# Kernel optimization log

Hardware: AMD Instinct MI355X
Metric: run time of the kernel (lower is better)

## Reference

```python
import jax, jax.numpy as jnp
import numpy as np

B, D, C, W, H = 2, 8, 256, 84, 84
NUM_HEADS = 8
WS = (2, 7, 7)
SS = (1, 3, 3)
MLP_RATIO = 4
EPS = 1e-5


def _rel_pos_index(ws):
    # static int index table (N, N), matches WindowAttention3D buffer
    coords = np.stack(np.meshgrid(np.arange(ws[0]), np.arange(ws[1]), np.arange(ws[2]), indexing='ij'))
    cf = coords.reshape(3, -1)
    rel = (cf[:, :, None] - cf[:, None, :]).transpose(1, 2, 0).copy()
    rel[:, :, 0] += ws[0] - 1
    rel[:, :, 1] += ws[1] - 1
    rel[:, :, 2] += ws[2] - 1
    rel[:, :, 0] *= (2 * ws[1] - 1) * (2 * ws[2] - 1)
    rel[:, :, 1] *= 2 * ws[2] - 1
    return rel.sum(-1)


def _attn_mask(Dp, Hp, Wp, ws, ss):
    # static additive shift mask (nW, N, N), matches create_mask
    m = np.zeros((Dp, Hp, Wp))
    cnt = 0
    for d in (slice(0, -ws[0]), slice(-ws[0], -ss[0]), slice(-ss[0], None)):
        for h in (slice(0, -ws[1]), slice(-ws[1], -ss[1]), slice(-ss[1], None)):
            for w in (slice(0, -ws[2]), slice(-ws[2], -ss[2]), slice(-ss[2], None)):
                m[d, h, w] = cnt
                cnt += 1
    mw = m.reshape(Dp // ws[0], ws[0], Hp // ws[1], ws[1], Wp // ws[2], ws[2])
    mw = mw.transpose(0, 2, 4, 1, 3, 5).reshape(-1, ws[0] * ws[1] * ws[2])
    diff = mw[:, None, :] - mw[:, :, None]
    return np.where(diff != 0, -100.0, 0.0).astype(np.float32)


def _layernorm(x, g, b):
    mu = x.mean(-1, keepdims=True)
    var = ((x - mu) ** 2).mean(-1, keepdims=True)
    return (x - mu) * jax.lax.rsqrt(var + EPS) * g + b


def setup_inputs():
    key = jax.random.key(0)
    ks = jax.random.split(key, 6)
    hidden = C * MLP_RATIO
    nbias = (2 * WS[0] - 1) * (2 * WS[1] - 1) * (2 * WS[2] - 1)
    s = lambda k, shape, sc=0.02: jax.random.normal(k, shape, jnp.float32) * sc
    return dict(
        x=jax.random.normal(ks[0], (B, D, C, W, H), jnp.float32),
        norm1_g=jnp.ones((C,), jnp.float32), norm1_b=jnp.zeros((C,), jnp.float32),
        qkv_w=s(ks[1], (3 * C, C)),
        rpb_table=s(ks[2], (nbias, NUM_HEADS)),
        proj_w=s(ks[3], (C, C)), proj_b=jnp.zeros((C,), jnp.float32),
        norm2_g=jnp.ones((C,), jnp.float32), norm2_b=jnp.zeros((C,), jnp.float32),
        fc1_w=s(ks[4], (hidden, C)), fc1_b=jnp.zeros((hidden,), jnp.float32),
        fc2_w=s(ks[5], (C, hidden)), fc2_b=jnp.zeros((C,), jnp.float32),
    )


def reference(x, norm1_g, norm1_b, qkv_w, rpb_table, proj_w, proj_b,
              norm2_g, norm2_b, fc1_w, fc1_b, fc2_w, fc2_b):
    # x: (B, D, C, W, H) -> (B, D, H, W, C)
    xp = jnp.transpose(x, (0, 1, 4, 3, 2))
    Bn, Dn, Hn, Wn, Cn = xp.shape
    wd, wh, ww = WS
    N = wd * wh * ww
    nW = (Dn // wd) * (Hn // wh) * (Wn // ww)
    head_dim = Cn // NUM_HEADS
    scale = head_dim ** -0.5

    rel_idx = _rel_pos_index(WS)                      # (N, N) static
    mask = jnp.asarray(_attn_mask(Dn, Hn, Wn, WS, SS))  # (nW, N, N) static

    shortcut = xp
    h1 = _layernorm(xp, norm1_g, norm1_b)
    # cyclic shift (D,H,W divisible by window -> no padding)
    h1 = jnp.roll(h1, shift=(-SS[0], -SS[1], -SS[2]), axis=(1, 2, 3))
    # window partition -> (B*nW, N, C)
    xw = h1.reshape(Bn, Dn // wd, wd, Hn // wh, wh, Wn // ww, ww, Cn)
    xw = jnp.transpose(xw, (0, 1, 3, 5, 2, 4, 6, 7)).reshape(-1, N, Cn)
    B_ = xw.shape[0]

    qkv = (xw @ qkv_w.T).reshape(B_, N, 3, NUM_HEADS, head_dim)
    qkv = jnp.transpose(qkv, (2, 0, 3, 1, 4))  # (3, B_, h, N, hd)
    q, k, v = qkv[0] * scale, qkv[1], qkv[2]
    attn = jnp.einsum('bhnd,bhmd->bhnm', q, k)
    bias = rpb_table[rel_idx.reshape(-1)].reshape(N, N, NUM_HEADS)
    attn = attn + jnp.transpose(bias, (2, 0, 1))[None]
    attn = attn.reshape(Bn, nW, NUM_HEADS, N, N) + mask[None, :, None]
    attn = jax.nn.softmax(attn.reshape(B_, NUM_HEADS, N, N), axis=-1)
    out = jnp.einsum('bhnm,bhmd->bhnd', attn, v)
    out = jnp.transpose(out, (0, 2, 1, 3)).reshape(B_, N, Cn)
    out = out @ proj_w.T + proj_b

    # window reverse -> (B, D, H, W, C)
    out = out.reshape(Bn, Dn // wd, Hn // wh, Wn // ww, wd, wh, ww, Cn)
    out = jnp.transpose(out, (0, 1, 4, 2, 5, 3, 6, 7)).reshape(Bn, Dn, Hn, Wn, Cn)
    out = jnp.roll(out, shift=(SS[0], SS[1], SS[2]), axis=(1, 2, 3))

    xres = shortcut + out
    # MLP block (torch GELU = exact erf)
    h2 = _layernorm(xres, norm2_g, norm2_b)
    h2 = jax.nn.gelu(h2 @ fc1_w.T + fc1_b, approximate=False)
    h2 = h2 @ fc2_w.T + fc2_b
    y = xres + h2
    return jnp.transpose(y, (0, 1, 4, 3, 2))  # back to (B, D, C, W, H)
```

## Files before the change

kernel.cpp:

```cpp
#include <hip/hip_runtime.h>
#include <hip/hip_bf16.h>
#include <cstdint>
#include <cstddef>

#define B_   2
#define D_   8
#define C_   256
#define W_   84
#define H_   84
#define NH   8
#define HD   32
#define NTOK 98
#define WH   7056
#define M2   56448
#define NWC  576

typedef __attribute__((ext_vector_type(8))) short sh8;
typedef __attribute__((ext_vector_type(4))) float f32x4;
typedef __hip_bfloat16 bf16;

#define AS1 __attribute__((address_space(1)))
#define AS3 __attribute__((address_space(3)))

__global__ __launch_bounds__(256) void k_f2b(const float* __restrict__ in,
                                             bf16* __restrict__ out, int n) {
  int i = blockIdx.x * 256 + threadIdx.x;
  if (i < n) out[i] = __float2bfloat16(in[i]);
}

__global__ __launch_bounds__(256) void k_bias(const float* __restrict__ rpb,
                                              float* __restrict__ tbl) {
  int cls = blockIdx.x >> 3, h = blockIdx.x & 7;
  int dB = cls >> 2, hB = (cls >> 1) & 1, wB = cls & 1;
  for (int idx = threadIdx.x; idx < 112 * 112; idx += 256) {
    int r = idx / 112, c = idx - (idx / 112) * 112;
    int rt = r < 98 ? r : 97, ct = c < 98 ? c : 97;
    int jdr = rt / 49, remr = rt % 49, jhr = remr / 7, jwr = remr % 7;
    int jdc = ct / 49, remc = ct % 49, jhc = remc / 7, jwc = remc % 7;
    int bir = jdr * 169 + jhr * 13 + jwr, bic = jdc * 169 + jhc * 13 + jwc;
    int dgr = dB ? ((6 + jdr) < 7 ? 1 : 2) : 0;
    int hgr = hB ? ((77 + jhr) < 81 ? 1 : 2) : 0;
    int wgr = wB ? ((77 + jwr) < 81 ? 1 : 2) : 0;
    int dgc = dB ? ((6 + jdc) < 7 ? 1 : 2) : 0;
    int hgc = hB ? ((77 + jhc) < 81 ? 1 : 2) : 0;
    int wgc = wB ? ((77 + jwc) < 81 ? 1 : 2) : 0;
    int cir = dgr * 9 + hgr * 3 + wgr, cic = dgc * 9 + hgc * 3 + wgc;
    float v = rpb[(bir - bic + 253) * 8 + h] + (cir == cic ? 0.f : -100.f);
    tbl[((size_t)(cls * 8 + h) * 112 + r) * 112 + c] = v;
  }
}

__device__ __forceinline__ int inv_row(int b, int d0, int w0, int h0) {
  int sd = (d0 + 7) & 7;
  int lid = (sd >> 1) & 1, jd = sd & 1;
  int sh = h0 + 81; if (sh >= 84) sh -= 84;
  int sw = w0 + 81; if (sw >= 84) sw -= 84;
  int ih = sh / 7, jh = sh - ih * 7;
  int iw = sw / 7, jw = sw - iw * 7;
  return (b * 288 + lid * 144 + ih * 12 + iw) * 98 + jd * 49 + jh * 7 + jw;
}

__global__ __launch_bounds__(256) void k_xpose_w(const float* __restrict__ x,
                                                 float* __restrict__ xtw, int cchunk) {
  int blk = blockIdx.x;
  int ch = blk & 1;
  int t = blk >> 1;
  int w0 = t % 84;
  int t2 = t / 84;
  int i = t2 & 3, b = t2 >> 2;
  int d0 = (cchunk * 4 + 1 + i) & 7;
  __shared__ float tile[128][85];
  __shared__ int rtab[84];
  int tid = threadIdx.x;
  if (tid < 84) rtab[tid] = inv_row(b, d0, w0, tid);
  const float* src = x + ((size_t)(b * 8 + d0) * 256 + ch * 128) * WH + w0 * 84;
  for (int idx = tid; idx < 128 * 21; idx += 256) {
    int c = idx / 21, h4 = idx - c * 21;
    float4 v = *(const float4*)(src + (size_t)c * WH + h4 * 4);
    tile[c][h4 * 4 + 0] = v.x; tile[c][h4 * 4 + 1] = v.y;
    tile[c][h4 * 4 + 2] = v.z; tile[c][h4 * 4 + 3] = v.w;
  }
  __syncthreads();
  for (int idx = tid; idx < 84 * 128; idx += 256) {
    int h = idx >> 7, cc = idx & 127;
    xtw[(size_t)rtab[h] * 256 + ch * 128 + cc] = tile[cc][h];
  }
}

__global__ __launch_bounds__(256) void k_ln1_lin(
    const float* __restrict__ xtw, const float* __restrict__ g,
    const float* __restrict__ bb, bf16* __restrict__ xw) {
  int rl = blockIdx.x * 4 + (threadIdx.x >> 6);
  int lane = threadIdx.x & 63;
  int c0 = lane * 4;
  float4 v = *(const float4*)(xtw + (size_t)rl * 256 + c0);
  float s = v.x + v.y + v.z + v.w;
  float s2 = v.x * v.x + v.y * v.y + v.z * v.z + v.w * v.w;
#pragma unroll
  for (int off = 32; off; off >>= 1) { s += __shfl_xor(s, off, 64); s2 += __shfl_xor(s2, off, 64); }
  float mu = s * (1.f / 256.f);
  float var = s2 * (1.f / 256.f) - mu * mu;
  float rs = rsqrtf(var + 1e-5f);
  float4 gg = *(const float4*)(g + c0);
  float4 bv = *(const float4*)(bb + c0);
  bf16 tmp[4];
  tmp[0] = __float2bfloat16((v.x - mu) * rs * gg.x + bv.x);
  tmp[1] = __float2bfloat16((v.y - mu) * rs * gg.y + bv.y);
  tmp[2] = __float2bfloat16((v.z - mu) * rs * gg.z + bv.z);
  tmp[3] = __float2bfloat16((v.w - mu) * rs * gg.w + bv.w);
  *(ushort4*)(&xw[(size_t)rl * 256 + c0]) = *(ushort4*)tmp;
}

__device__ __forceinline__ float gelu_fast(float v) {
  float x = v * 0.70710678118f;
  float ax = fabsf(x);
  float t = 1.0f / (1.0f + 0.3275911f * ax);
  float y = t * (0.254829592f + t * (-0.284496736f +
            t * (1.421413741f + t * (-1.453152027f + t * 1.061405429f))));
  float er = 1.0f - y * __expf(-ax * ax);
  er = copysignf(er, x);
  return 0.5f * v * (1.0f + er);
}

template <int EPI, int NK>
__global__ __launch_bounds__(256) void k_gemm_bt(
    const bf16* __restrict__ A, const bf16* __restrict__ Bw,
    int M, int N,
    const float* __restrict__ bias, const float* __restrict__ res,
    void* __restrict__ outv) {
  constexpr int K = NK * 32;
  __shared__ __align__(16) short smem[16384];
  int nwg = gridDim.x;
  int orig = blockIdx.x;
  int q8 = nwg >> 3, r8 = nwg & 7;
  int xcd = orig & 7, lwg = orig >> 3;
  int bid = (xcd < r8 ? xcd * (q8 + 1) : r8 * (q8 + 1) + (xcd - r8) * q8) + lwg;
  int nbn = N >> 7;
  int bm = bid / nbn, bn = bid - bm * nbn;
  int tid = threadIdx.x;
  int lane = tid & 63, wv = tid >> 6;
  int wr = wv >> 1, wc = wv & 1;
  f32x4 acc[4][4] = {};
  const short* Ag = (const short*)A + (size_t)bm * 128 * K;
  const short* Bg = (const short*)Bw + (size_t)bn * 128 * K;
  int rIn = lane >> 2;
  int cSrc = ((lane & 3) ^ ((lane >> 3) & 3)) * 8;
  const short* gA0 = Ag + (size_t)(wv * 32 + rIn) * K + cSrc;
  const short* gA1 = gA0 + 16 * K;
  const short* gB0 = Bg + (size_t)(wv * 32 + rIn) * K + cSrc;
  const short* gB1 = gB0 + 16 * K;
  const int ldsW = wv * 1024;
  int rb = wr * 64 + (lane & 15);
  int cb = wc * 64 + (lane & 15);
  int kswz = ((lane >> 4) ^ ((lane >> 1) & 3)) * 8;
  const short* rdA = smem + rb * 32 + kswz;
  const short* rdB = smem + 4096 + cb * 32 + kswz;

  __builtin_amdgcn_global_load_lds((const AS1 void*)gA0, (AS3 void*)&smem[ldsW], 16, 0, 0);
  __builtin_amdgcn_global_load_lds((const AS1 void*)gA1, (AS3 void*)&smem[ldsW + 512], 16, 0, 0);
  __builtin_amdgcn_global_load_lds((const AS1 void*)gB0, (AS3 void*)&smem[4096 + ldsW], 16, 0, 0);
  __builtin_amdgcn_global_load_lds((const AS1 void*)gB1, (AS3 void*)&smem[4096 + ldsW + 512], 16, 0, 0);

#pragma unroll
  for (int kt = 0; kt < NK; ++kt) {
    const int buf = kt & 1;
    __builtin_amdgcn_s_barrier();
    if (kt + 1 < NK) {
      const int wb = (buf ^ 1) * 8192;
      __builtin_amdgcn_global_load_lds((const AS1 void*)(gA0 + (kt + 1) * 32),
                                       (AS3 void*)&smem[wb + ldsW], 16, 0, 0);
      __builtin_amdgcn_global_load_lds((const AS1 void*)(gA1 + (kt + 1) * 32),
                                       (AS3 void*)&smem[wb + ldsW + 512], 16, 0, 0);
      __builtin_amdgcn_global_load_lds((const AS1 void*)(gB0 + (kt + 1) * 32),
                                       (AS3 void*)&smem[wb + 4096 + ldsW], 16, 0, 0);
      __builtin_amdgcn_global_load_lds((const AS1 void*)(gB1 + (kt + 1) * 32),
                                       (AS3 void*)&smem[wb + 4096 + ldsW + 512], 16, 0, 0);
      asm volatile("s_waitcnt vmcnt(4)" ::: "memory");
    } else {
      asm volatile("s_waitcnt vmcnt(0)" ::: "memory");
    }
    __builtin_amdgcn_s_barrier();
    __builtin_amdgcn_sched_barrier(0);
    sh8 af[4], bfr[4];
#pragma unroll
    for (int m = 0; m < 4; ++m) af[m] = *(const sh8*)(rdA + buf * 8192 + m * 512);
#pragma unroll
    for (int n2 = 0; n2 < 4; ++n2) bfr[n2] = *(const sh8*)(rdB + buf * 8192 + n2 * 512);
    __builtin_amdgcn_s_setprio(1);
#pragma unroll
    for (int m = 0; m < 4; ++m)
#pragma unroll
      for (int n2 = 0; n2 < 4; ++n2)
        acc[m][n2] = __builtin_amdgcn_mfma_f32_16x16x32_bf16(af[m], bfr[n2], acc[m][n2], 0, 0, 0);
    __builtin_amdgcn_s_setprio(0);
  }
  int rbase = bm * 128 + wr * 64 + ((lane >> 4) << 2);
  int cbase = bn * 128 + wc * 64 + (lane & 15);
#pragma unroll
  for (int m = 0; m < 4; ++m) {
#pragma unroll
    for (int j = 0; j < 4; ++j) {
      int r = rbase + m * 16 + j;
#pragma unroll
      for (int n2 = 0; n2 < 4; ++n2) {
        int cc = cbase + n2 * 16;
        float v = acc[m][n2][j];
        if (EPI == 2) {
          v += bias[cc] + res[(size_t)r * N + cc];
          ((float*)outv)[(size_t)r * N + cc] = v;
        } else {
          if (bias) v += bias[cc];
          if (EPI == 1) v = gelu_fast(v);
          ((bf16*)outv)[(size_t)r * N + cc] = __float2bfloat16(v);
        }
      }
    }
  }
}

__global__ __launch_bounds__(64) void k_attn_mfma(
    const bf16* __restrict__ qkv, const float* __restrict__ tbl,
    bf16* __restrict__ aout, int idbase) {
  int blk = blockIdx.x;
  int wl = blk >> 3, h = blk & 7;
  int lid = (wl / 144) & 1;
  int id = idbase + lid;
  int rem = wl % 144;
  int ih = rem / 12, iw = rem - ih * 12;
  int cls = ((id == 3) ? 4 : 0) + ((ih == 11) ? 2 : 0) + ((iw == 11) ? 1 : 0);
  const float* bt = tbl + (size_t)(cls * 8 + h) * 112 * 112;
  int lane = threadIdx.x;
  __shared__ __align__(16) short vt[32][136];
  __shared__ __align__(16) short pb[16][136];
  sh8 z = {};
  for (int i = lane; i < 544; i += 64) *((sh8*)&vt[0][0] + i) = z;
  for (int i = lane; i < 272; i += 64) *((sh8*)&pb[0][0] + i) = z;
  __syncthreads();
  const size_t base = (size_t)wl * NTOK * 768;
  for (int i = lane; i < 98 * 8; i += 64) {
    int c = i >> 3, d4 = (i & 7) * 4;
    ushort4 vu = *(const ushort4*)&qkv[base + (size_t)c * 768 + 512 + h * 32 + d4];
    vt[d4 + 0][c] = (short)vu.x; vt[d4 + 1][c] = (short)vu.y;
    vt[d4 + 2][c] = (short)vu.z; vt[d4 + 3][c] = (short)vu.w;
  }
  int kq = (lane >> 4) * 8;
  sh8 kf[7];
#pragma unroll
  for (int jt = 0; jt < 7; ++jt) {
    int c = jt * 16 + (lane & 15);
    kf[jt] = *(const sh8*)&qkv[base + (size_t)c * 768 + 256 + h * 32 + kq];
  }
  __syncthreads();
  sh8 vb[2][4];
#pragma unroll
  for (int dt = 0; dt < 2; ++dt)
#pragma unroll
    for (int k2 = 0; k2 < 4; ++k2)
      vb[dt][k2] = *(const sh8*)&vt[dt * 16 + (lane & 15)][k2 * 32 + kq];

  const float scale = 0.17677669529663687f;
  f32x4 zc = {};
  int rband = (lane >> 4) * 4;
  for (int it = 0; it < 7; ++it) {
    int rq = it * 16 + (lane & 15);
    sh8 qf = *(const sh8*)&qkv[base + (size_t)rq * 768 + h * 32 + kq];
    f32x4 s[7];
#pragma unroll
    for (int jt = 0; jt < 7; ++jt)
      s[jt] = __builtin_amdgcn_mfma_f32_16x16x32_bf16(qf, kf[jt], zc, 0, 0, 0);
    float p[7][4], linv[4];
#pragma unroll
    for (int j = 0; j < 4; ++j) {
      int r2 = it * 16 + rband + j;
      float rs = 0.f;
#pragma unroll
      for (int jt = 0; jt < 7; ++jt) {
        int c = jt * 16 + (lane & 15);
        float v = s[jt][j] * scale + bt[r2 * 112 + c];
        float e = __expf(v);
        if (jt == 6 && (lane & 15) >= 2) e = 0.f;
        p[jt][j] = e;
        rs += e;
      }
      rs += __shfl_xor(rs, 1, 64); rs += __shfl_xor(rs, 2, 64);
      rs += __shfl_xor(rs, 4, 64); rs += __shfl_xor(rs, 8, 64);
      linv[j] = 1.f / rs;
    }
#pragma unroll
    for (int j = 0; j < 4; ++j)
#pragma unroll
      for (int jt = 0; jt < 7; ++jt) {
        bf16 bv = __float2bfloat16(p[jt][j] * linv[j]);
        pb[rband + j][jt * 16 + (lane & 15)] = *(short*)&bv;
      }
    __syncthreads();
    sh8 pa[4];
#pragma unroll
    for (int k2 = 0; k2 < 4; ++k2)
      pa[k2] = *(const sh8*)&pb[lane & 15][k2 * 32 + kq];
    f32x4 o[2] = {};
#pragma unroll
    for (int dt = 0; dt < 2; ++dt)
#pragma unroll
      for (int k2 = 0; k2 < 4; ++k2)
        o[dt] = __builtin_amdgcn_mfma_f32_16x16x32_bf16(pa[k2], vb[dt][k2], o[dt], 0, 0, 0);
#pragma unroll
    for (int j = 0; j < 4; ++j) {
      int r2 = it * 16 + rband + j;
      if (r2 < 98) {
#pragma unroll
        for (int dt = 0; dt < 2; ++dt) {
          bf16 ov = __float2bfloat16(o[dt][j]);
          aout[((size_t)wl * 98 + r2) * 256 + h * 32 + dt * 16 + (lane & 15)] = ov;
        }
      }
    }
    __syncthreads();
  }
}

__global__ __launch_bounds__(256) void k_xres_ln2_lin(
    const float* __restrict__ xtw, const bf16* __restrict__ pout,
    const float* __restrict__ g, const float* __restrict__ bb,
    float* __restrict__ xres, bf16* __restrict__ ln2) {
  int rl = blockIdx.x * 4 + (threadIdx.x >> 6);
  int lane = threadIdx.x & 63;
  int c0 = lane * 4;
  float4 v = *(const float4*)(xtw + (size_t)rl * 256 + c0);
  ushort4 pu = *(const ushort4*)(pout + (size_t)rl * 256 + c0);
  v.x += __bfloat162float(*(bf16*)&pu.x);
  v.y += __bfloat162float(*(bf16*)&pu.y);
  v.z += __bfloat162float(*(bf16*)&pu.z);
  v.w += __bfloat162float(*(bf16*)&pu.w);
  *(float4*)(xres + (size_t)rl * 256 + c0) = v;
  float s = v.x + v.y + v.z + v.w;
  float s2 = v.x * v.x + v.y * v.y + v.z * v.z + v.w * v.w;
#pragma unroll
  for (int off = 32; off; off >>= 1) { s += __shfl_xor(s, off, 64); s2 += __shfl_xor(s2, off, 64); }
  float mu = s * (1.f / 256.f);
  float var = s2 * (1.f / 256.f) - mu * mu;
  float rs = rsqrtf(var + 1e-5f);
  float4 gg = *(const float4*)(g + c0);
  float4 bv = *(const float4*)(bb + c0);
  bf16 tmp[4];
  tmp[0] = __float2bfloat16((v.x - mu) * rs * gg.x + bv.x);
  tmp[1] = __float2bfloat16((v.y - mu) * rs * gg.y + bv.y);
  tmp[2] = __float2bfloat16((v.z - mu) * rs * gg.z + bv.z);
  tmp[3] = __float2bfloat16((v.w - mu) * rs * gg.w + bv.w);
  *(ushort4*)(&ln2[(size_t)rl * 256 + c0]) = *(ushort4*)tmp;
}

__global__ __launch_bounds__(256) void k_final_c(const float* __restrict__ y,
                                                 float* __restrict__ out, int cchunk) {
  int t = blockIdx.x;
  int w0 = t % 84;
  int t2 = t / 84;
  int i = t2 & 3, b = t2 >> 2;
  int d0 = (cchunk * 4 + 1 + i) & 7;
  __shared__ float tile[84][65];
  __shared__ int rtab[84];
  int tid = threadIdx.x;
  if (tid < 84) rtab[tid] = inv_row(b, d0, w0, tid);
  __syncthreads();
  for (int c0 = 0; c0 < 256; c0 += 64) {
    for (int idx = tid; idx < 84 * 64; idx += 256) {
      int hh = idx >> 6, cc = idx & 63;
      tile[hh][cc] = y[(size_t)rtab[hh] * 256 + c0 + cc];
    }
    __syncthreads();
    for (int idx = tid; idx < 64 * 84; idx += 256) {
      int cc = idx / 84, hh = idx - cc * 84;
      out[((((size_t)b * 8 + d0) * 256 + c0 + cc) * 84 + w0) * 84 + hh] = tile[hh][cc];
    }
    __syncthreads();
  }
}

extern "C" void kernel_launch(void* const* d_in, const int* in_sizes, int n_in,
                              void* d_out, int out_size, void* d_ws, size_t ws_size,
                              hipStream_t stream) {
  const float* x      = (const float*)d_in[0];
  const float* n1g    = (const float*)d_in[1];
  const float* n1b    = (const float*)d_in[2];
  const float* qkv_w  = (const float*)d_in[3];
  const float* rpb    = (const float*)d_in[4];
  const float* proj_w = (const float*)d_in[5];
  const float* proj_b = (const float*)d_in[6];
  const float* n2g    = (const float*)d_in[7];
  const float* n2b    = (const float*)d_in[8];
  const float* fc1_w  = (const float*)d_in[9];
  const float* fc1_b  = (const float*)d_in[10];
  const float* fc2_w  = (const float*)d_in[11];
  const float* fc2_b  = (const float*)d_in[12];
  float* out = (float*)d_out;

  char* w = (char*)d_ws;
  size_t off = 0;
  bf16* wq = (bf16*)(w + off); off += (size_t)768 * 256 * 2;
  bf16* wp = (bf16*)(w + off); off += (size_t)256 * 256 * 2;
  bf16* w1 = (bf16*)(w + off); off += (size_t)1024 * 256 * 2;
  bf16* w2 = (bf16*)(w + off); off += (size_t)1024 * 256 * 2;
  float* tbl = (float*)(w + off); off += (size_t)8 * 8 * 112 * 112 * 4;

  float* xtw  = (float*)(w + off); off += (size_t)M2 * 1024;
  bf16*  xw   = (bf16*)(w + off);  off += (size_t)M2 * 512;
  char*  qreg = w + off;           off += (size_t)M2 * 1536;
  float* xres = (float*)(w + off); off += (size_t)M2 * 1024;
  bf16*  hid  = (bf16*)(w + off);
  bf16* qkvb = (bf16*)qreg;
  bf16* aout = xw;
  bf16* pout = (bf16*)qreg;
  bf16* ln2b = (bf16*)(qreg + (size_t)M2 * 512);
  float* ybuf = xtw;

  int subTiles = 21;
  if (off + (size_t)441 * 128 * 2048 + 1024 <= ws_size) subTiles = 441;
  else if (off + (size_t)147 * 128 * 2048 + 1024 <= ws_size) subTiles = 147;
  else if (off + (size_t)49 * 128 * 2048 + 1024 <= ws_size) subTiles = 49;
  const int nsub = 441 / subTiles;
  const int MSUB = subTiles * 128;

  k_f2b<<<(196608 + 255) / 256, 256, 0, stream>>>(qkv_w, wq, 196608);
  k_f2b<<<(65536 + 255) / 256, 256, 0, stream>>>(proj_w, wp, 65536);
  k_f2b<<<(262144 + 255) / 256, 256, 0, stream>>>(fc1_w, w1, 262144);
  k_f2b<<<(262144 + 255) / 256, 256, 0, stream>>>(fc2_w, w2, 262144);
  k_bias<<<64, 256, 0, stream>>>(rpb, tbl);

  for (int c = 0; c < 2; ++c) {
    k_xpose_w<<<1344, 256, 0, stream>>>(x, xtw, c);
    k_ln1_lin<<<M2 / 4, 256, 0, stream>>>(xtw, n1g, n1b, xw);
    k_gemm_bt<0, 8><<<441 * 6, 256, 0, stream>>>(xw, wq, M2, 768, nullptr, nullptr, qkvb);
    k_attn_mfma<<<NWC * NH, 64, 0, stream>>>(qkvb, tbl, aout, 2 * c);
    k_gemm_bt<0, 8><<<441 * 2, 256, 0, stream>>>(aout, wp, M2, 256, proj_b, nullptr, pout);
    k_xres_ln2_lin<<<M2 / 4, 256, 0, stream>>>(xtw, pout, n2g, n2b, xres, ln2b);
    for (int s = 0; s < nsub; ++s) {
      size_t m0 = (size_t)s * MSUB;
      k_gemm_bt<1, 8><<<subTiles * 8, 256, 0, stream>>>(
          ln2b + m0 * 256, w1, MSUB, 1024, fc1_b, nullptr, hid);
      k_gemm_bt<2, 32><<<subTiles * 2, 256, 0, stream>>>(
          hid, w2, MSUB, 256, fc2_b, xres + m0 * 256, ybuf + m0 * 256);
    }
    k_final_c<<<672, 256, 0, stream>>>(ybuf, out, c);
  }
}
```

Baseline: 841.5 us.

## Add 128x256-tile 512-thread GEMM for QKV and FC1 projections

Introduces a new GEMM kernel using 512 threads (8 waves) with a 128x256 output tile, double-buffered direct global-to-LDS loads, swizzled LDS reads and XCD-aware block remapping. It replaces the older 128-wide-N GEMM for the QKV and FC1 projections so each A tile is reused across twice as many output columns, halving the number of A reloads. The larger tile raises LDS use to 48KB and register pressure, which may lower occupancy.

```diff
diff --git a/kernel.cpp b/kernel.cpp
--- a/kernel.cpp
+++ b/kernel.cpp
@@ -218,6 +218,94 @@
   }
 }
 
+template <int EPI, int NK>
+__global__ __launch_bounds__(512) void k_gemm_w(
+    const bf16* __restrict__ A, const bf16* __restrict__ Bw,
+    int M, int N,
+    const float* __restrict__ bias, const float* __restrict__ res,
+    void* __restrict__ outv) {
+  constexpr int K = NK * 32;
+  __shared__ __align__(16) short smem[24576];
+  int nwg = gridDim.x;
+  int orig = blockIdx.x;
+  int q8 = nwg >> 3, r8 = nwg & 7;
+  int xcd = orig & 7, lwg = orig >> 3;
+  int bid = (xcd < r8 ? xcd * (q8 + 1) : r8 * (q8 + 1) + (xcd - r8) * q8) + lwg;
+  int nbn = N >> 8;
+  int bm = bid / nbn, bn = bid - bm * nbn;
+  int tid = threadIdx.x;
+  int lane = tid & 63, wv = tid >> 6;
+  int wr = wv >> 2, wc = wv & 3;
+  f32x4 acc[4][4] = {};
+  const short* Ag = (const short*)A + (size_t)bm * 128 * K;
+  const short* Bg = (const short*)Bw + (size_t)bn * 256 * K;
+  int rIn = lane >> 2;
+  int cSrc = ((lane & 3) ^ ((lane >> 3) & 3)) * 8;
+  const short* gA0 = Ag + (size_t)(wv * 16 + rIn) * K + cSrc;
+  const short* gB0 = Bg + (size_t)(wv * 32 + rIn) * K + cSrc;
+  const short* gB1 = gB0 + 16 * K;
+  const int ldsA = wv * 512;
+  const int ldsB = 4096 + wv * 1024;
+  int rb = wr * 64 + (lane & 15);
+  int cb = wc * 64 + (lane & 15);
+  int kswz = ((lane >> 4) ^ ((lane >> 1) & 3)) * 8;
+  const short* rdA = smem + rb * 32 + kswz;
+  const short* rdB = smem + 4096 + cb * 32 + kswz;
+
+  __builtin_amdgcn_global_load_lds((const AS1 void*)gA0, (AS3 void*)&smem[ldsA], 16, 0, 0);
+  __builtin_amdgcn_global_load_lds((const AS1 void*)gB0, (AS3 void*)&smem[ldsB], 16, 0, 0);
+  __builtin_amdgcn_global_load_lds((const AS1 void*)gB1, (AS3 void*)&smem[ldsB + 512], 16, 0, 0);
+
+#pragma unroll
+  for (int kt = 0; kt < NK; ++kt) {
+    const int buf = kt & 1;
+    __builtin_amdgcn_s_barrier();
+    if (kt + 1 < NK) {
+      const int wb = (buf ^ 1) * 12288;
+      __builtin_amdgcn_global_load_lds((const AS1 void*)(gA0 + (kt + 1) * 32),
+                                       (AS3 void*)&smem[wb + ldsA], 16, 0, 0);
+      __builtin_amdgcn_global_load_lds((const AS1 void*)(gB0 + (kt + 1) * 32),
+                                       (AS3 void*)&smem[wb + ldsB], 16, 0, 0);
+      __builtin_amdgcn_global_load_lds((const AS1 void*)(gB1 + (kt + 1) * 32),
+                                       (AS3 void*)&smem[wb + ldsB + 512], 16, 0, 0);
+      asm volatile("s_waitcnt vmcnt(3)" ::: "memory");
+    } else {
+      asm volatile("s_waitcnt vmcnt(0)" ::: "memory");
+    }
+    __builtin_amdgcn_s_barrier();
+    __builtin_amdgcn_sched_barrier(0);
+    sh8 af[4], bfr[4];
+#pragma unroll
+    for (int m = 0; m < 4; ++m) af[m] = *(const sh8*)(rdA + buf * 12288 + m * 512);
+#pragma unroll
+    for (int n2 = 0; n2 < 4; ++n2) bfr[n2] = *(const sh8*)(rdB + buf * 12288 + n2 * 512);
+    __builtin_amdgcn_s_setprio(1);
+#pragma unroll
+    for (int m = 0; m < 4; ++m)
+#pragma unroll
+      for (int n2 = 0; n2 < 4; ++n2)
+        acc[m][n2] = __builtin_amdgcn_mfma_f32_16x16x32_bf16(af[m], bfr[n2], acc[m][n2], 0, 0, 0);
+    __builtin_amdgcn_s_setprio(0);
+  }
+  int rbase = bm * 128 + wr * 64 + ((lane >> 4) << 2);
+  int cbase = bn * 256 + wc * 64 + (lane & 15);
+#pragma unroll
+  for (int m = 0; m < 4; ++m) {
+#pragma unroll
+    for (int j = 0; j < 4; ++j) {
+      int r = rbase + m * 16 + j;
+#pragma unroll
+      for (int n2 = 0; n2 < 4; ++n2) {
+        int cc = cbase + n2 * 16;
+        float v = acc[m][n2][j];
+        if (bias) v += bias[cc];
+        if (EPI == 1) v = gelu_fast(v);
+        ((bf16*)outv)[(size_t)r * N + cc] = __float2bfloat16(v);
+      }
+    }
+  }
+}
+
 __global__ __launch_bounds__(64) void k_attn_mfma(
     const bf16* __restrict__ qkv, const float* __restrict__ tbl,
     bf16* __restrict__ aout, int idbase) {
@@ -429,15 +517,15 @@
   for (int c = 0; c < 2; ++c) {
     k_xpose_w<<<1344, 256, 0, stream>>>(x, xtw, c);
     k_ln1_lin<<<M2 / 4, 256, 0, stream>>>(xtw, n1g, n1b, xw);
-    k_gemm_bt<0, 8><<<441 * 6, 256, 0, stream>>>(xw, wq, M2, 768, nullptr, nullptr, qkvb);
+    k_gemm_w<0, 8><<<441 * 3, 512, 0, stream>>>(xw, wq, M2, 768, nullptr, nullptr, qkvb);
     k_attn_mfma<<<NWC * NH, 64, 0, stream>>>(qkvb, tbl, aout, 2 * c);
     k_gemm_bt<0, 8><<<441 * 2, 256, 0, stream>>>(aout, wp, M2, 256, proj_b, nullptr, pout);
     k_xres_ln2_lin<<<M2 / 4, 256, 0, stream>>>(xtw, pout, n2g, n2b, xres, ln2b);
     for (int s = 0; s < nsub; ++s) {
       size_t m0 = (size_t)s * MSUB;
-      k_gemm_bt<1, 8><<<subTiles * 8, 256, 0, stream>>>(
+      k_gemm_w<1, 8><<<(MSUB / 128) * 4, 512, 0, stream>>>(
           ln2b + m0 * 256, w1, MSUB, 1024, fc1_b, nullptr, hid);
-      k_gemm_bt<2, 32><<<subTiles * 2, 256, 0, stream>>>(
+      k_gemm_bt<2, 32><<<(MSUB / 128) * 2, 256, 0, stream>>>(
           hid, w2, MSUB, 256, fc2_b, xres + m0 * 256, ybuf + m0 * 256);
     }
     k_final_c<<<672, 256, 0, stream>>>(ybuf, out, c);
```

New measurement: 822.1 us. -2.3%, faster.
